# Optimization experiments

Hardware: AMD Instinct MI355X
Metric: run time of the kernel (lower is better)

Reference implementation:

```python
import jax, jax.numpy as jnp
import numpy as np


def conv1x1(x, W, b):
    # 1x1 Conv2d == per-pixel linear over channels. x: [B,C,H,W], W: [O,C], b: [O]
    return jnp.einsum('oc,bchw->bohw', W, x) + b[None, :, None, None]


def setup_inputs() -> dict:
    key = jax.random.key(0)
    ks = jax.random.split(key, 18)
    B, C, Hd, H, W = 16, 64, 64, 32, 32
    s = 0.05
    f = jax.random.normal
    return {
        'h': f(ks[0], (B, C, H, W), jnp.float32),
        'm': f(ks[1], (B, C, H, W), jnp.float32),
        'Wq': f(ks[2], (Hd, C), jnp.float32) * s,
        'bq': f(ks[3], (Hd,), jnp.float32) * s,
        'Wk': f(ks[4], (Hd, C), jnp.float32) * s,
        'bk': f(ks[5], (Hd,), jnp.float32) * s,
        'Wk2': f(ks[6], (Hd, C), jnp.float32) * s,
        'bk2': f(ks[7], (Hd,), jnp.float32) * s,
        'Wv': f(ks[8], (C, C), jnp.float32) * s,
        'bv': f(ks[9], (C,), jnp.float32) * s,
        'Wv2': f(ks[10], (C, C), jnp.float32) * s,
        'bv2': f(ks[11], (C,), jnp.float32) * s,
        'Wz': f(ks[12], (2 * C, 2 * C), jnp.float32) * s,
        'bz': f(ks[13], (2 * C,), jnp.float32) * s,
        'Wm': f(ks[14], (3 * C, 3 * C), jnp.float32) * s,
        'bm': f(ks[15], (3 * C,), jnp.float32) * s,
    }


def reference(h, m, Wq, bq, Wk, bk, Wk2, bk2, Wv, bv, Wv2, bv2, Wz, bz, Wm, bm):
    B, C, H, W = h.shape
    Hd = Wq.shape[0]
    N = H * W
    # Shared query from h
    Q_h = conv1x1(h, Wq, bq).reshape(B, Hd, N).transpose(0, 2, 1)  # [B,N,Hd]
    # Self-attention branch over h
    K_h = conv1x1(h, Wk, bk).reshape(B, Hd, N)                     # [B,Hd,N]
    A_h = jax.nn.softmax(jnp.einsum('bnd,bdm->bnm', Q_h, K_h), axis=-1)  # [B,N,N]
    V_h = conv1x1(h, Wv, bv).reshape(B, C, N)                      # [B,C,N]
    Z_h = jnp.einsum('bnm,bcm->bcn', A_h, V_h).reshape(B, C, H, W)
    # Cross-attention branch over memory m (same query Q_h)
    K_m = conv1x1(m, Wk2, bk2).reshape(B, Hd, N)
    A_m = jax.nn.softmax(jnp.einsum('bnd,bdm->bnm', Q_h, K_m), axis=-1)
    V_m = conv1x1(m, Wv2, bv2).reshape(B, C, N)
    Z_m = jnp.einsum('bnm,bcm->bcn', A_m, V_m).reshape(B, C, H, W)
    # Fuse and gated memory update
    Z = conv1x1(jnp.concatenate([Z_h, Z_m], axis=1), Wz, bz)       # [B,2C,H,W]
    combined = conv1x1(jnp.concatenate([Z, h], axis=1), Wm, bm)    # [B,3C,H,W]
    mo, mg, mi = combined[:, :C], combined[:, C:2 * C], combined[:, 2 * C:]
    mi = jax.nn.sigmoid(mi)
    new_m = (1 - mi) * m + mi * jnp.tanh(mg)
    new_h = jax.nn.sigmoid(mo) * new_m
    return (new_h, new_m)
```

## Files before the change

kernel.cpp:

```cpp
#include <hip/hip_runtime.h>

typedef unsigned short u16;
typedef unsigned int u32;
typedef __attribute__((ext_vector_type(8))) short bf16x8;
typedef __attribute__((ext_vector_type(4))) float f32x4;

#define MFMA(a, b, c) __builtin_amdgcn_mfma_f32_16x16x32_bf16((a), (b), (c), 0, 0, 0)

static __device__ __forceinline__ u16 f2bf(float x) {
  u32 u = __float_as_uint(x);
  u += 0x7FFFu + ((u >> 16) & 1u);
  return (u16)(u >> 16);
}
static __device__ __forceinline__ u32 packbf_t(float hi, float lo) {
  return __builtin_amdgcn_perm(__float_as_uint(hi), __float_as_uint(lo), 0x07060302u);
}
static __device__ __forceinline__ u32 packbf(float lo, float hi) {
  return (u32)f2bf(lo) | ((u32)f2bf(hi) << 16);
}

__global__ void prep_kernel(const float* __restrict__ Wq, const float* __restrict__ Wk,
                            const float* __restrict__ Wk2, const float* __restrict__ Wv,
                            const float* __restrict__ Wv2, const float* __restrict__ Wz,
                            const float* __restrict__ Wm, const float* __restrict__ bm,
                            u16* __restrict__ W5, u16* __restrict__ Wzb,
                            u16* __restrict__ Wmb, float* __restrict__ bmp) {
  const int id = blockIdx.x * 256 + threadIdx.x;
  if (id < 20480) {
    const int wi = id >> 12, e = id & 4095;
    const float* src = wi == 0 ? Wq : wi == 1 ? Wk : wi == 2 ? Wk2 : wi == 3 ? Wv : Wv2;
    W5[id] = f2bf(src[e]);
  } else if (id < 36864) {
    const int e = id - 20480;
    Wzb[e] = f2bf(Wz[e]);
  } else if (id < 73728) {
    const int e = id - 36864;
    const int p = e / 192, k = e % 192;
    const int hb2 = p / 96, r1 = p % 96, ctl = r1 / 48, r2 = r1 % 48;
    const int g = r2 >> 4, mm = r2 & 15;
    const int o = g * 64 + (hb2 * 2 + ctl) * 16 + mm;
    Wmb[p * 192 + k] = f2bf(Wm[o * 192 + k]);
  } else if (id < 73920) {
    const int p = id - 73728;
    const int hb2 = p / 96, r1 = p % 96, ctl = r1 / 48, r2 = r1 % 48;
    const int g = r2 >> 4, mm = r2 & 15;
    const int o = g * 64 + (hb2 * 2 + ctl) * 16 + mm;
    bmp[p] = bm[o];
  }
}

__global__ __launch_bounds__(256) void proj_kernel(
    const float* __restrict__ h, const float* __restrict__ m_,
    const float* __restrict__ bq, const float* __restrict__ bk,
    const float* __restrict__ bk2, const float* __restrict__ bv,
    const float* __restrict__ bv2, const u16* __restrict__ W5,
    u16* __restrict__ Qb, u16* __restrict__ Khb, u16* __restrict__ Kmb,
    u16* __restrict__ Vhb, u16* __restrict__ Vmb, u16* __restrict__ hbuf)
{
  const int b = blockIdx.y, n0 = blockIdx.x * 64, z = blockIdx.z;
  __shared__ __align__(16) u16 xt[64][72];
  const int tid = threadIdx.x;
  const float* __restrict__ X = z ? m_ : h;

  {
    const int px = tid & 63, c0 = (tid >> 6) * 16;
#pragma unroll
    for (int i = 0; i < 8; ++i) {
      const int c = c0 + 2 * i;
      const float f0 = X[(b * 64 + c) * 1024 + n0 + px];
      const float f1 = X[(b * 64 + c + 1) * 1024 + n0 + px];
      *(u32*)&xt[px][c] = packbf(f0, f1);
    }
  }
  __syncthreads();

  const int lane = tid & 63, w = tid >> 6;
  const int mm = lane & 15, q = lane >> 4;

  const bf16x8 xa0 = *(const bf16x8*)&xt[w * 16 + mm][q * 8];
  const bf16x8 xa1 = *(const bf16x8*)&xt[w * 16 + mm][32 + q * 8];

  auto qk_store = [&](u16* dst, const u16* Wb, const float* bias) {
#pragma unroll
    for (int ot = 0; ot < 4; ++ot) {
      const bf16x8 wb0 = *(const bf16x8*)(Wb + (ot * 16 + mm) * 64 + q * 8);
      const bf16x8 wb1 = *(const bf16x8*)(Wb + (ot * 16 + mm) * 64 + 32 + q * 8);
      const float4 b4 = *(const float4*)(bias + ot * 16 + q * 4);
      f32x4 d = {b4.x, b4.y, b4.z, b4.w};
      d = MFMA(wb0, xa0, d);
      d = MFMA(wb1, xa1, d);
      uint2 val;
      val.x = packbf(d[0], d[1]);
      val.y = packbf(d[2], d[3]);
      *(uint2*)(dst + (b * 1024 + n0 + w * 16 + mm) * 64 + ot * 16 + q * 4) = val;
    }
  };
  auto v_store = [&](u16* dst, const u16* Wb, const float* bias) {
#pragma unroll
    for (int ot = 0; ot < 4; ++ot) {
      const bf16x8 wb0 = *(const bf16x8*)(Wb + (ot * 16 + mm) * 64 + q * 8);
      const bf16x8 wb1 = *(const bf16x8*)(Wb + (ot * 16 + mm) * 64 + 32 + q * 8);
      const float bb = bias[ot * 16 + mm];
      f32x4 d = {bb, bb, bb, bb};
      d = MFMA(xa0, wb0, d);
      d = MFMA(xa1, wb1, d);
      uint2 val;
      val.x = packbf(d[0], d[1]);
      val.y = packbf(d[2], d[3]);
      *(uint2*)(dst + (b * 64 + ot * 16 + mm) * 1024 + n0 + w * 16 + q * 4) = val;
    }
  };

  if (z == 0) {
    qk_store(Qb, W5, bq);
    qk_store(Khb, W5 + 4096, bk);
    v_store(Vhb, W5 + 3 * 4096, bv);
    const int px = tid >> 2, sg = tid & 3;
    u32* dst = (u32*)(hbuf + (b * 1024 + n0 + px) * 64 + sg * 16);
    const u16* srcr = &xt[px][sg * 16];
#pragma unroll
    for (int j = 0; j < 8; ++j) dst[j] = *(const u32*)(srcr + 2 * j);
  } else {
    qk_store(Kmb, W5 + 2 * 4096, bk2);
    v_store(Vmb, W5 + 4 * 4096, bv2);
  }
}

__global__ __launch_bounds__(256, 4) void attn_kernel(
    const u16* __restrict__ Qb, const u16* __restrict__ Khb,
    const u16* __restrict__ Kmb, const u16* __restrict__ Vhb,
    const u16* __restrict__ Vmb, u16* __restrict__ Ztb)
{
  const int id = blockIdx.x;
  const int b = id & 15, rest = id >> 4;
  const int br = rest & 1, qb0 = (rest >> 1) * 32;
  const u16* __restrict__ K = br ? Kmb : Khb;
  const u16* __restrict__ V = br ? Vmb : Vhb;

  __shared__ __align__(16) u16 zcb[4][32][68];
  __shared__ float rsw[4][32];

  const int tid = threadIdx.x, w = tid >> 6, lane = tid & 63;
  const int mm = lane & 15, q = lane >> 4;

  bf16x8 qa0[2], qa1[2];
#pragma unroll
  for (int qt = 0; qt < 2; ++qt) {
    const u16* Qp = Qb + (b * 1024 + qb0 + qt * 16 + mm) * 64;
    qa0[qt] = *(const bf16x8*)(Qp + q * 8);
    qa1[qt] = *(const bf16x8*)(Qp + 32 + q * 8);
  }

  f32x4 z[2][4];
#pragma unroll
  for (int qt = 0; qt < 2; ++qt)
#pragma unroll
    for (int ct = 0; ct < 4; ++ct) z[qt][ct] = (f32x4){0.f, 0.f, 0.f, 0.f};
  float rp[2] = {0.f, 0.f};

  const int kb0 = w * 256;
  const int base = (2 * (q & 1)) * 16 + mm;
  const bool hiq = q >= 2;

  for (int ch = 0; ch < 8; ++ch) {
    const int kb = kb0 + ch * 32;
    bf16x8 kf0[2], kf1[2], vf[4];
#pragma unroll
    for (int t = 0; t < 2; ++t) {
      const u16* Kp = K + (b * 1024 + kb + t * 16 + mm) * 64;
      kf0[t] = *(const bf16x8*)(Kp + q * 8);
      kf1[t] = *(const bf16x8*)(Kp + 32 + q * 8);
    }
#pragma unroll
    for (int ct = 0; ct < 4; ++ct)
      vf[ct] = *(const bf16x8*)(V + (b * 64 + ct * 16 + mm) * 1024 + kb + q * 8);

#pragma unroll
    for (int qt = 0; qt < 2; ++qt) {
      u32 P0, P1, P2, P3;
      {
        f32x4 s = {0.f, 0.f, 0.f, 0.f};
        s = MFMA(kf0[0], qa0[qt], s);
        s = MFMA(kf1[0], qa1[qt], s);
        const float e0 = __expf(s[0]), e1 = __expf(s[1]);
        const float e2 = __expf(s[2]), e3 = __expf(s[3]);
        rp[qt] += (e0 + e1) + (e2 + e3);
        P0 = packbf_t(e1, e0);
        P1 = packbf_t(e3, e2);
      }
      {
        f32x4 s = {0.f, 0.f, 0.f, 0.f};
        s = MFMA(kf0[1], qa0[qt], s);
        s = MFMA(kf1[1], qa1[qt], s);
        const float e0 = __expf(s[0]), e1 = __expf(s[1]);
        const float e2 = __expf(s[2]), e3 = __expf(s[3]);
        rp[qt] += (e0 + e1) + (e2 + e3);
        P2 = packbf_t(e1, e0);
        P3 = packbf_t(e3, e2);
      }
      const u32 l0 = (u32)__shfl((int)P0, base),      h0 = (u32)__shfl((int)P2, base);
      const u32 l1 = (u32)__shfl((int)P1, base),      h1 = (u32)__shfl((int)P3, base);
      const u32 l2 = (u32)__shfl((int)P0, base + 16), h2 = (u32)__shfl((int)P2, base + 16);
      const u32 l3 = (u32)__shfl((int)P1, base + 16), h3 = (u32)__shfl((int)P3, base + 16);
      union { u32 u[4]; bf16x8 v; } bu;
      bu.u[0] = hiq ? h0 : l0;
      bu.u[1] = hiq ? h1 : l1;
      bu.u[2] = hiq ? h2 : l2;
      bu.u[3] = hiq ? h3 : l3;
#pragma unroll
      for (int ct = 0; ct < 4; ++ct) z[qt][ct] = MFMA(vf[ct], bu.v, z[qt][ct]);
    }
  }

#pragma unroll
  for (int qt = 0; qt < 2; ++qt) {
#pragma unroll
    for (int ct = 0; ct < 4; ++ct) {
      uint2 val;
      val.x = packbf_t(z[qt][ct][1], z[qt][ct][0]);
      val.y = packbf_t(z[qt][ct][3], z[qt][ct][2]);
      *(uint2*)&zcb[w][qt * 16 + mm][ct * 16 + q * 4] = val;
    }
    float v = rp[qt];
    v += __shfl_xor(v, 16);
    v += __shfl_xor(v, 32);
    if (q == 0) rsw[w][qt * 16 + mm] = v;
  }
  __syncthreads();

  const int c2 = tid & 31, q0 = tid >> 5;
#pragma unroll
  for (int i = 0; i < 4; ++i) {
    const int query = q0 + i * 8;
    const float rt = rsw[0][query] + rsw[1][query] + rsw[2][query] + rsw[3][query];
    const float rinv = __builtin_amdgcn_rcpf(rt);
    float vlo = 0.f, vhi = 0.f;
#pragma unroll
    for (int ww = 0; ww < 4; ++ww) {
      const u32 u = *(const u32*)&zcb[ww][query][c2 * 2];
      vlo += __uint_as_float(u << 16);
      vhi += __uint_as_float(u & 0xffff0000u);
    }
    vlo *= rinv;
    vhi *= rinv;
    *(u32*)(Ztb + (b * 1024 + qb0 + query) * 128 + br * 64 + c2 * 2) = packbf_t(vhi, vlo);
  }
}

__global__ __launch_bounds__(256) void tail_kernel(
    const u16* __restrict__ Ztb, const u16* __restrict__ hbuf,
    const float* __restrict__ m_, const u16* __restrict__ Wzb,
    const float* __restrict__ bz, const u16* __restrict__ Wmb,
    const float* __restrict__ bmp, float* __restrict__ out)
{
  const int b = blockIdx.y, n0 = blockIdx.x * 32;
  __shared__ __align__(16) u16 zp[32][136];
  const int tid = threadIdx.x, lane = tid & 63, wv = tid >> 6;
  const int mm = lane & 15, q = lane >> 4;
  const int pxt = wv & 1, oh = wv >> 1;

  {
    bf16x8 za[4];
#pragma unroll
    for (int ks = 0; ks < 4; ++ks)
      za[ks] = *(const bf16x8*)(Ztb + (b * 1024 + n0 + pxt * 16 + mm) * 128 +
                                ks * 32 + q * 8);
#pragma unroll
    for (int ot = 0; ot < 4; ++ot) {
      const int o0 = oh * 64 + ot * 16;
      const float4 b4 = *(const float4*)(bz + o0 + q * 4);
      f32x4 d = {b4.x, b4.y, b4.z, b4.w};
#pragma unroll
      for (int ks = 0; ks < 4; ++ks) {
        const bf16x8 wb = *(const bf16x8*)(Wzb + (o0 + mm) * 128 + ks * 32 + q * 8);
        d = MFMA(wb, za[ks], d);
      }
      uint2 val;
      val.x = packbf(d[0], d[1]);
      val.y = packbf(d[2], d[3]);
      *(uint2*)&zp[pxt * 16 + mm][o0 + q * 4] = val;
    }
  }
  __syncthreads();

  {
    const int hb2 = oh;
    bf16x8 fa[6];
#pragma unroll
    for (int ks = 0; ks < 4; ++ks)
      fa[ks] = *(const bf16x8*)&zp[pxt * 16 + mm][ks * 32 + q * 8];
    {
      const u16* hp = hbuf + (b * 1024 + n0 + pxt * 16 + mm) * 64;
      fa[4] = *(const bf16x8*)(hp + q * 8);
      fa[5] = *(const bf16x8*)(hp + 32 + q * 8);
    }
    f32x4 dd[6];
#pragma unroll
    for (int j = 0; j < 6; ++j) {
      const int p = hb2 * 96 + j * 16 + mm;
      const float bb = bmp[p];
      f32x4 d = {bb, bb, bb, bb};
#pragma unroll
      for (int ks = 0; ks < 6; ++ks) {
        const bf16x8 wb = *(const bf16x8*)(Wmb + p * 192 + ks * 32 + q * 8);
        d = MFMA(fa[ks], wb, d);
      }
      dd[j] = d;
    }
#pragma unroll
    for (int ctl = 0; ctl < 2; ++ctl) {
      const int c = (hb2 * 2 + ctl) * 16 + mm;
      const int px = n0 + pxt * 16 + q * 4;
      const float4 mold = *(const float4*)(m_ + (b * 64 + c) * 1024 + px);
      float4 nh, nm;
#pragma unroll
      for (int r = 0; r < 4; ++r) {
        const float xo = dd[ctl * 3 + 0][r];
        const float xg = dd[ctl * 3 + 1][r];
        const float xi = dd[ctl * 3 + 2][r];
        const float si = __builtin_amdgcn_rcpf(1.f + __expf(-xi));
        const float th = 1.f - 2.f * __builtin_amdgcn_rcpf(__expf(2.f * xg) + 1.f);
        const float so = __builtin_amdgcn_rcpf(1.f + __expf(-xo));
        const float mo = ((const float*)&mold)[r];
        const float nmv = (1.f - si) * mo + si * th;
        ((float*)&nm)[r] = nmv;
        ((float*)&nh)[r] = so * nmv;
      }
      *(float4*)(out + (b * 64 + c) * 1024 + px) = nh;
      *(float4*)(out + 1048576 + (b * 64 + c) * 1024 + px) = nm;
    }
  }
}

extern "C" void kernel_launch(void* const* d_in, const int* in_sizes, int n_in,
                              void* d_out, int out_size, void* d_ws, size_t ws_size,
                              hipStream_t stream) {
  const float* h   = (const float*)d_in[0];
  const float* m   = (const float*)d_in[1];
  const float* Wq  = (const float*)d_in[2];
  const float* bq  = (const float*)d_in[3];
  const float* Wk  = (const float*)d_in[4];
  const float* bk  = (const float*)d_in[5];
  const float* Wk2 = (const float*)d_in[6];
  const float* bk2 = (const float*)d_in[7];
  const float* Wv  = (const float*)d_in[8];
  const float* bv  = (const float*)d_in[9];
  const float* Wv2 = (const float*)d_in[10];
  const float* bv2 = (const float*)d_in[11];
  const float* Wz  = (const float*)d_in[12];
  const float* bz  = (const float*)d_in[13];
  const float* Wm  = (const float*)d_in[14];
  const float* bm  = (const float*)d_in[15];
  float* out = (float*)d_out;

  char* ws = (char*)d_ws;
  const size_t MB = 1024 * 1024;
  u16* Qb   = (u16*)(ws + 0 * MB);
  u16* Khb  = (u16*)(ws + 2 * MB);
  u16* Kmb  = (u16*)(ws + 4 * MB);
  u16* Vhb  = (u16*)(ws + 6 * MB);
  u16* Vmb  = (u16*)(ws + 8 * MB);
  u16* hbuf = (u16*)(ws + 10 * MB);
  u16* Ztb  = (u16*)(ws + 12 * MB);
  u16* W5   = (u16*)(ws + 16 * MB);
  u16* Wzb  = (u16*)(ws + 16 * MB + 40960);
  u16* Wmb  = (u16*)(ws + 16 * MB + 73728);
  float* bmp = (float*)(ws + 16 * MB + 147456);

  prep_kernel<<<289, 256, 0, stream>>>(Wq, Wk, Wk2, Wv, Wv2, Wz, Wm, bm,
                                       W5, Wzb, Wmb, bmp);
  proj_kernel<<<dim3(16, 16, 2), 256, 0, stream>>>(h, m, bq, bk, bk2, bv, bv2, W5,
                                                   Qb, Khb, Kmb, Vhb, Vmb, hbuf);
  attn_kernel<<<1024, 256, 0, stream>>>(Qb, Khb, Kmb, Vhb, Vmb, Ztb);
  tail_kernel<<<dim3(32, 16), 256, 0, stream>>>(Ztb, hbuf, m, Wzb, bz, Wmb, bmp, out);
}
```

Baseline: 157.7 us.

## Give each attention wave full key range and double-buffer K/V chunk loads

The attention kernel used to split the key range across four waves and combine partial results through shared memory with a block barrier. Now each wave owns 16 queries and walks all 1024 keys, so the LDS reduction and __syncthreads go away and the output is normalised and written straight from registers. K/V fragments are software-pipelined with two register chunks so loads overlap the MFMA and exp work. In exchange, K/V loads per query are less shared (one query tile per wave instead of two), the grid halves to 512 blocks, and the occupancy hint is dropped, which may change register allocation.

Result: slower. 178.4 us (+13.1%).

```diff
diff --git a/kernel.cpp b/kernel.cpp
--- a/kernel.cpp
+++ b/kernel.cpp
@@ -126,124 +126,102 @@
   }
 }
 
-__global__ __launch_bounds__(256, 4) void attn_kernel(
+struct Chunk { bf16x8 f[8]; };
+
+__global__ __launch_bounds__(256) void attn_kernel(
     const u16* __restrict__ Qb, const u16* __restrict__ Khb,
     const u16* __restrict__ Kmb, const u16* __restrict__ Vhb,
     const u16* __restrict__ Vmb, u16* __restrict__ Ztb)
 {
   const int id = blockIdx.x;
-  const int b = id & 15, rest = id >> 4;
-  const int br = rest & 1, qb0 = (rest >> 1) * 32;
+  const int b = id & 15;
+  const int br = (id >> 4) & 1;
+  const int qt = id >> 5;
   const u16* __restrict__ K = br ? Kmb : Khb;
   const u16* __restrict__ V = br ? Vmb : Vhb;
 
-  __shared__ __align__(16) u16 zcb[4][32][68];
-  __shared__ float rsw[4][32];
-
   const int tid = threadIdx.x, w = tid >> 6, lane = tid & 63;
   const int mm = lane & 15, q = lane >> 4;
-
-  bf16x8 qa0[2], qa1[2];
-#pragma unroll
-  for (int qt = 0; qt < 2; ++qt) {
-    const u16* Qp = Qb + (b * 1024 + qb0 + qt * 16 + mm) * 64;
-    qa0[qt] = *(const bf16x8*)(Qp + q * 8);
-    qa1[qt] = *(const bf16x8*)(Qp + 32 + q * 8);
-  }
-
-  f32x4 z[2][4];
-#pragma unroll
-  for (int qt = 0; qt < 2; ++qt)
-#pragma unroll
-    for (int ct = 0; ct < 4; ++ct) z[qt][ct] = (f32x4){0.f, 0.f, 0.f, 0.f};
-  float rp[2] = {0.f, 0.f};
-
-  const int kb0 = w * 256;
+  const int q0 = qt * 64 + w * 16;
+
+  const u16* Qp = Qb + (b * 1024 + q0 + mm) * 64;
+  const bf16x8 qa0 = *(const bf16x8*)(Qp + q * 8);
+  const bf16x8 qa1 = *(const bf16x8*)(Qp + 32 + q * 8);
+
+  f32x4 z[4];
+#pragma unroll
+  for (int ct = 0; ct < 4; ++ct) z[ct] = (f32x4){0.f, 0.f, 0.f, 0.f};
+  float rp = 0.f;
+
   const int base = (2 * (q & 1)) * 16 + mm;
   const bool hiq = q >= 2;
 
-  for (int ch = 0; ch < 8; ++ch) {
-    const int kb = kb0 + ch * 32;
-    bf16x8 kf0[2], kf1[2], vf[4];
-#pragma unroll
-    for (int t = 0; t < 2; ++t) {
-      const u16* Kp = K + (b * 1024 + kb + t * 16 + mm) * 64;
-      kf0[t] = *(const bf16x8*)(Kp + q * 8);
-      kf1[t] = *(const bf16x8*)(Kp + 32 + q * 8);
-    }
+  auto loadch = [&](int kb, Chunk& c) {
+    const u16* Kp0 = K + (b * 1024 + kb + mm) * 64;
+    c.f[0] = *(const bf16x8*)(Kp0 + q * 8);
+    c.f[1] = *(const bf16x8*)(Kp0 + 32 + q * 8);
+    c.f[2] = *(const bf16x8*)(Kp0 + 1024 + q * 8);
+    c.f[3] = *(const bf16x8*)(Kp0 + 1024 + 32 + q * 8);
 #pragma unroll
     for (int ct = 0; ct < 4; ++ct)
-      vf[ct] = *(const bf16x8*)(V + (b * 64 + ct * 16 + mm) * 1024 + kb + q * 8);
-
-#pragma unroll
-    for (int qt = 0; qt < 2; ++qt) {
-      u32 P0, P1, P2, P3;
-      {
-        f32x4 s = {0.f, 0.f, 0.f, 0.f};
-        s = MFMA(kf0[0], qa0[qt], s);
-        s = MFMA(kf1[0], qa1[qt], s);
-        const float e0 = __expf(s[0]), e1 = __expf(s[1]);
-        const float e2 = __expf(s[2]), e3 = __expf(s[3]);
-        rp[qt] += (e0 + e1) + (e2 + e3);
-        P0 = packbf_t(e1, e0);
-        P1 = packbf_t(e3, e2);
-      }
-      {
-        f32x4 s = {0.f, 0.f, 0.f, 0.f};
-        s = MFMA(kf0[1], qa0[qt], s);
-        s = MFMA(kf1[1], qa1[qt], s);
-        const float e0 = __expf(s[0]), e1 = __expf(s[1]);
-        const float e2 = __expf(s[2]), e3 = __expf(s[3]);
-        rp[qt] += (e0 + e1) + (e2 + e3);
-        P2 = packbf_t(e1, e0);
-        P3 = packbf_t(e3, e2);
-      }
-      const u32 l0 = (u32)__shfl((int)P0, base),      h0 = (u32)__shfl((int)P2, base);
-      const u32 l1 = (u32)__shfl((int)P1, base),      h1 = (u32)__shfl((int)P3, base);
-      const u32 l2 = (u32)__shfl((int)P0, base + 16), h2 = (u32)__shfl((int)P2, base + 16);
-      const u32 l3 = (u32)__shfl((int)P1, base + 16), h3 = (u32)__shfl((int)P3, base + 16);
-      union { u32 u[4]; bf16x8 v; } bu;
-      bu.u[0] = hiq ? h0 : l0;
-      bu.u[1] = hiq ? h1 : l1;
-      bu.u[2] = hiq ? h2 : l2;
-      bu.u[3] = hiq ? h3 : l3;
-#pragma unroll
-      for (int ct = 0; ct < 4; ++ct) z[qt][ct] = MFMA(vf[ct], bu.v, z[qt][ct]);
-    }
-  }
-
-#pragma unroll
-  for (int qt = 0; qt < 2; ++qt) {
-#pragma unroll
-    for (int ct = 0; ct < 4; ++ct) {
-      uint2 val;
-      val.x = packbf_t(z[qt][ct][1], z[qt][ct][0]);
-      val.y = packbf_t(z[qt][ct][3], z[qt][ct][2]);
-      *(uint2*)&zcb[w][qt * 16 + mm][ct * 16 + q * 4] = val;
-    }
-    float v = rp[qt];
-    v += __shfl_xor(v, 16);
-    v += __shfl_xor(v, 32);
-    if (q == 0) rsw[w][qt * 16 + mm] = v;
-  }
-  __syncthreads();
-
-  const int c2 = tid & 31, q0 = tid >> 5;
-#pragma unroll
-  for (int i = 0; i < 4; ++i) {
-    const int query = q0 + i * 8;
-    const float rt = rsw[0][query] + rsw[1][query] + rsw[2][query] + rsw[3][query];
-    const float rinv = __builtin_amdgcn_rcpf(rt);
-    float vlo = 0.f, vhi = 0.f;
-#pragma unroll
-    for (int ww = 0; ww < 4; ++ww) {
-      const u32 u = *(const u32*)&zcb[ww][query][c2 * 2];
-      vlo += __uint_as_float(u << 16);
-      vhi += __uint_as_float(u & 0xffff0000u);
-    }
-    vlo *= rinv;
-    vhi *= rinv;
-    *(u32*)(Ztb + (b * 1024 + qb0 + query) * 128 + br * 64 + c2 * 2) = packbf_t(vhi, vlo);
+      c.f[4 + ct] = *(const bf16x8*)(V + (b * 64 + ct * 16 + mm) * 1024 + kb + q * 8);
+  };
+
+  auto compute = [&](const Chunk& c) {
+    u32 P0, P1, P2, P3;
+    {
+      f32x4 s = {0.f, 0.f, 0.f, 0.f};
+      s = MFMA(c.f[0], qa0, s);
+      s = MFMA(c.f[1], qa1, s);
+      const float e0 = __expf(s[0]), e1 = __expf(s[1]);
+      const float e2 = __expf(s[2]), e3 = __expf(s[3]);
+      rp += (e0 + e1) + (e2 + e3);
+      P0 = packbf_t(e1, e0);
+      P1 = packbf_t(e3, e2);
+    }
+    {
+      f32x4 s = {0.f, 0.f, 0.f, 0.f};
+      s = MFMA(c.f[2], qa0, s);
+      s = MFMA(c.f[3], qa1, s);
+      const float e0 = __expf(s[0]), e1 = __expf(s[1]);
+      const float e2 = __expf(s[2]), e3 = __expf(s[3]);
+      rp += (e0 + e1) + (e2 + e3);
+      P2 = packbf_t(e1, e0);
+      P3 = packbf_t(e3, e2);
+    }
+    const u32 l0 = (u32)__shfl((int)P0, base),      h0 = (u32)__shfl((int)P2, base);
+    const u32 l1 = (u32)__shfl((int)P1, base),      h1 = (u32)__shfl((int)P3, base);
+    const u32 l2 = (u32)__shfl((int)P0, base + 16), h2 = (u32)__shfl((int)P2, base + 16);
+    const u32 l3 = (u32)__shfl((int)P1, base + 16), h3 = (u32)__shfl((int)P3, base + 16);
+    union { u32 u[4]; bf16x8 v; } bu;
+    bu.u[0] = hiq ? h0 : l0;
+    bu.u[1] = hiq ? h1 : l1;
+    bu.u[2] = hiq ? h2 : l2;
+    bu.u[3] = hiq ? h3 : l3;
+#pragma unroll
+    for (int ct = 0; ct < 4; ++ct) z[ct] = MFMA(c.f[4 + ct], bu.v, z[ct]);
+  };
+
+  Chunk fA, fB;
+  loadch(0, fA);
+#pragma unroll 1
+  for (int cc = 0; cc < 16; ++cc) {
+    loadch(cc * 64 + 32, fB);
+    compute(fA);
+    if (cc < 15) loadch(cc * 64 + 64, fA);
+    compute(fB);
+  }
+
+  rp += __shfl_xor(rp, 16);
+  rp += __shfl_xor(rp, 32);
+  const float rinv = __builtin_amdgcn_rcpf(rp);
+  u16* Zr = Ztb + (b * 1024 + q0 + mm) * 128 + br * 64 + q * 4;
+#pragma unroll
+  for (int ct = 0; ct < 4; ++ct) {
+    uint2 val;
+    val.x = packbf(z[ct][0] * rinv, z[ct][1] * rinv);
+    val.y = packbf(z[ct][2] * rinv, z[ct][3] * rinv);
+    *(uint2*)(Zr + ct * 16) = val;
   }
 }
 
@@ -371,6 +349,6 @@
                                        W5, Wzb, Wmb, bmp);
   proj_kernel<<<dim3(16, 16, 2), 256, 0, stream>>>(h, m, bq, bk, bk2, bv, bv2, W5,
                                                    Qb, Khb, Kmb, Vhb, Vmb, hbuf);
-  attn_kernel<<<1024, 256, 0, stream>>>(Qb, Khb, Kmb, Vhb, Vmb, Ztb);
+  attn_kernel<<<512, 256, 0, stream>>>(Qb, Khb, Kmb, Vhb, Vmb, Ztb);
   tail_kernel<<<dim3(32, 16), 256, 0, stream>>>(Ztb, hbuf, m, Wzb, bz, Wmb, bmp, out);
 }
```

## Restructure attention to share K/V tiles via double-buffered LDS across query waves

Applied to the files above, without the earlier changes.

Attention blocks now give each wave its own 32 queries over the full key range, instead of splitting keys across waves and reducing partial sums through LDS at the end. K and V chunks of 64 keys are staged cooperatively into swizzled, double-buffered shared memory with register prefetch, so four waves reuse each loaded tile. The V projection layout is changed to key-chunk-major tiles to match, and P is transposed through a small LDS scratch instead of cross-lane shuffles. The grid drops from 1024 to 256 blocks, which lowers parallelism on the device and adds a barrier per chunk.

After: 141.7 us. 10.2% less time.

```diff
diff --git a/kernel.cpp b/kernel.cpp
--- a/kernel.cpp
+++ b/kernel.cpp
@@ -107,7 +107,8 @@
       uint2 val;
       val.x = packbf(d[0], d[1]);
       val.y = packbf(d[2], d[3]);
-      *(uint2*)(dst + (b * 64 + ot * 16 + mm) * 1024 + n0 + w * 16 + q * 4) = val;
+      *(uint2*)(dst + b * 65536 + blockIdx.x * 4096 + (ot * 16 + mm) * 64 +
+                w * 16 + q * 4) = val;
     }
   };
 
@@ -126,27 +127,30 @@
   }
 }
 
-__global__ __launch_bounds__(256, 4) void attn_kernel(
+__global__ __launch_bounds__(256) void attn_kernel(
     const u16* __restrict__ Qb, const u16* __restrict__ Khb,
     const u16* __restrict__ Kmb, const u16* __restrict__ Vhb,
     const u16* __restrict__ Vmb, u16* __restrict__ Ztb)
 {
   const int id = blockIdx.x;
-  const int b = id & 15, rest = id >> 4;
-  const int br = rest & 1, qb0 = (rest >> 1) * 32;
-  const u16* __restrict__ K = br ? Kmb : Khb;
-  const u16* __restrict__ V = br ? Vmb : Vhb;
-
-  __shared__ __align__(16) u16 zcb[4][32][68];
-  __shared__ float rsw[4][32];
+  const int b = id & 15;
+  const int br = (id >> 4) & 1;
+  const int qh = id >> 5;
+  const u16* __restrict__ K = (br ? Kmb : Khb) + b * 65536;
+  const u16* __restrict__ V = (br ? Vmb : Vhb) + b * 65536;
+
+  __shared__ __align__(16) u16 Kl[2][4096];
+  __shared__ __align__(16) u16 Vl[2][4096];
+  __shared__ __align__(16) u16 ps[4][16][40];
 
   const int tid = threadIdx.x, w = tid >> 6, lane = tid & 63;
-  const int mm = lane & 15, q = lane >> 4;
+  const int mm = lane & 15, q = lane >> 4, m7 = mm & 7;
+  const int q0 = qh * 128 + w * 32;
 
   bf16x8 qa0[2], qa1[2];
 #pragma unroll
   for (int qt = 0; qt < 2; ++qt) {
-    const u16* Qp = Qb + (b * 1024 + qb0 + qt * 16 + mm) * 64;
+    const u16* Qp = Qb + (b * 1024 + q0 + qt * 16 + mm) * 64;
     qa0[qt] = *(const bf16x8*)(Qp + q * 8);
     qa1[qt] = *(const bf16x8*)(Qp + 32 + q * 8);
   }
@@ -158,92 +162,93 @@
     for (int ct = 0; ct < 4; ++ct) z[qt][ct] = (f32x4){0.f, 0.f, 0.f, 0.f};
   float rp[2] = {0.f, 0.f};
 
-  const int kb0 = w * 256;
-  const int base = (2 * (q & 1)) * 16 + mm;
-  const bool hiq = q >= 2;
-
-  for (int ch = 0; ch < 8; ++ch) {
-    const int kb = kb0 + ch * 32;
-    bf16x8 kf0[2], kf1[2], vf[4];
-#pragma unroll
-    for (int t = 0; t < 2; ++t) {
-      const u16* Kp = K + (b * 1024 + kb + t * 16 + mm) * 64;
-      kf0[t] = *(const bf16x8*)(Kp + q * 8);
-      kf1[t] = *(const bf16x8*)(Kp + 32 + q * 8);
-    }
-#pragma unroll
-    for (int ct = 0; ct < 4; ++ct)
-      vf[ct] = *(const bf16x8*)(V + (b * 64 + ct * 16 + mm) * 1024 + kb + q * 8);
-
-#pragma unroll
-    for (int qt = 0; qt < 2; ++qt) {
-      u32 P0, P1, P2, P3;
-      {
-        f32x4 s = {0.f, 0.f, 0.f, 0.f};
-        s = MFMA(kf0[0], qa0[qt], s);
-        s = MFMA(kf1[0], qa1[qt], s);
-        const float e0 = __expf(s[0]), e1 = __expf(s[1]);
-        const float e2 = __expf(s[2]), e3 = __expf(s[3]);
-        rp[qt] += (e0 + e1) + (e2 + e3);
-        P0 = packbf_t(e1, e0);
-        P1 = packbf_t(e3, e2);
-      }
-      {
-        f32x4 s = {0.f, 0.f, 0.f, 0.f};
-        s = MFMA(kf0[1], qa0[qt], s);
-        s = MFMA(kf1[1], qa1[qt], s);
-        const float e0 = __expf(s[0]), e1 = __expf(s[1]);
-        const float e2 = __expf(s[2]), e3 = __expf(s[3]);
-        rp[qt] += (e0 + e1) + (e2 + e3);
-        P2 = packbf_t(e1, e0);
-        P3 = packbf_t(e3, e2);
-      }
-      const u32 l0 = (u32)__shfl((int)P0, base),      h0 = (u32)__shfl((int)P2, base);
-      const u32 l1 = (u32)__shfl((int)P1, base),      h1 = (u32)__shfl((int)P3, base);
-      const u32 l2 = (u32)__shfl((int)P0, base + 16), h2 = (u32)__shfl((int)P2, base + 16);
-      const u32 l3 = (u32)__shfl((int)P1, base + 16), h3 = (u32)__shfl((int)P3, base + 16);
-      union { u32 u[4]; bf16x8 v; } bu;
-      bu.u[0] = hiq ? h0 : l0;
-      bu.u[1] = hiq ? h1 : l1;
-      bu.u[2] = hiq ? h2 : l2;
-      bu.u[3] = hiq ? h3 : l3;
-#pragma unroll
-      for (int ct = 0; ct < 4; ++ct) z[qt][ct] = MFMA(vf[ct], bu.v, z[qt][ct]);
-    }
+  const int u0 = tid, u1 = 256 + tid;
+  const int l0 = (((u0 & ~7) | ((u0 ^ (u0 >> 3)) & 7))) * 8;
+  const int l1 = (((u1 & ~7) | ((u1 ^ (u1 >> 3)) & 7))) * 8;
+  uint4 sk0, sk1, sv0, sv1;
+
+  auto stage_load = [&](int kc) {
+    const u16* Ks = K + kc * 4096;
+    const u16* Vs = V + kc * 4096;
+    sk0 = *(const uint4*)(Ks + u0 * 8);
+    sk1 = *(const uint4*)(Ks + u1 * 8);
+    sv0 = *(const uint4*)(Vs + u0 * 8);
+    sv1 = *(const uint4*)(Vs + u1 * 8);
+  };
+  auto stage_store = [&](u16* Kd, u16* Vd) {
+    *(uint4*)(Kd + l0) = sk0;
+    *(uint4*)(Kd + l1) = sk1;
+    *(uint4*)(Vd + l0) = sv0;
+    *(uint4*)(Vd + l1) = sv1;
+  };
+
+  stage_load(0);
+  stage_store(Kl[0], Vl[0]);
+  __syncthreads();
+
+  const u16* Kcur = Kl[0];
+  const u16* Vcur = Vl[0];
+  u16* Knxt = Kl[1];
+  u16* Vnxt = Vl[1];
+
+#pragma unroll 1
+  for (int kc = 0; kc < 16; ++kc) {
+    if (kc < 15) stage_load(kc + 1);
+
+#pragma unroll
+    for (int t2 = 0; t2 < 2; ++t2) {
+      bf16x8 kf0[2], kf1[2], vf[4];
+#pragma unroll
+      for (int tt = 0; tt < 2; ++tt) {
+        const u16* Kb = Kcur + (t2 * 32 + tt * 16 + mm) * 64;
+        kf0[tt] = *(const bf16x8*)(Kb + ((q ^ m7) * 8));
+        kf1[tt] = *(const bf16x8*)(Kb + (((q + 4) ^ m7) * 8));
+      }
+#pragma unroll
+      for (int ct = 0; ct < 4; ++ct) {
+        const u16* Vb = Vcur + (ct * 16 + mm) * 64;
+        vf[ct] = *(const bf16x8*)(Vb + (((t2 * 4 + q) ^ m7) * 8));
+      }
+
+#pragma unroll
+      for (int qt = 0; qt < 2; ++qt) {
+#pragma unroll
+        for (int tt = 0; tt < 2; ++tt) {
+          f32x4 s = {0.f, 0.f, 0.f, 0.f};
+          s = MFMA(kf0[tt], qa0[qt], s);
+          s = MFMA(kf1[tt], qa1[qt], s);
+          const float e0 = __expf(s[0]), e1 = __expf(s[1]);
+          const float e2 = __expf(s[2]), e3 = __expf(s[3]);
+          rp[qt] += (e0 + e1) + (e2 + e3);
+          *(u32*)&ps[w][mm][tt * 16 + q * 4] = packbf_t(e1, e0);
+          *(u32*)&ps[w][mm][tt * 16 + q * 4 + 2] = packbf_t(e3, e2);
+        }
+        const bf16x8 pb = *(const bf16x8*)&ps[w][mm][q * 8];
+#pragma unroll
+        for (int ct = 0; ct < 4; ++ct) z[qt][ct] = MFMA(vf[ct], pb, z[qt][ct]);
+      }
+    }
+
+    if (kc < 15) stage_store(Knxt, Vnxt);
+    __syncthreads();
+    const u16* tk = Kcur; Kcur = Knxt; Knxt = (u16*)tk;
+    const u16* tv = Vcur; Vcur = Vnxt; Vnxt = (u16*)tv;
   }
 
 #pragma unroll
   for (int qt = 0; qt < 2; ++qt) {
-#pragma unroll
-    for (int ct = 0; ct < 4; ++ct) {
-      uint2 val;
-      val.x = packbf_t(z[qt][ct][1], z[qt][ct][0]);
-      val.y = packbf_t(z[qt][ct][3], z[qt][ct][2]);
-      *(uint2*)&zcb[w][qt * 16 + mm][ct * 16 + q * 4] = val;
-    }
     float v = rp[qt];
     v += __shfl_xor(v, 16);
     v += __shfl_xor(v, 32);
-    if (q == 0) rsw[w][qt * 16 + mm] = v;
-  }
-  __syncthreads();
-
-  const int c2 = tid & 31, q0 = tid >> 5;
-#pragma unroll
-  for (int i = 0; i < 4; ++i) {
-    const int query = q0 + i * 8;
-    const float rt = rsw[0][query] + rsw[1][query] + rsw[2][query] + rsw[3][query];
-    const float rinv = __builtin_amdgcn_rcpf(rt);
-    float vlo = 0.f, vhi = 0.f;
-#pragma unroll
-    for (int ww = 0; ww < 4; ++ww) {
-      const u32 u = *(const u32*)&zcb[ww][query][c2 * 2];
-      vlo += __uint_as_float(u << 16);
-      vhi += __uint_as_float(u & 0xffff0000u);
-    }
-    vlo *= rinv;
-    vhi *= rinv;
-    *(u32*)(Ztb + (b * 1024 + qb0 + query) * 128 + br * 64 + c2 * 2) = packbf_t(vhi, vlo);
+    const float rinv = __builtin_amdgcn_rcpf(v);
+    u16* Zr = Ztb + (b * 1024 + q0 + qt * 16 + mm) * 128 + br * 64;
+#pragma unroll
+    for (int ct = 0; ct < 4; ++ct) {
+      uint2 val;
+      val.x = packbf(z[qt][ct][0] * rinv, z[qt][ct][1] * rinv);
+      val.y = packbf(z[qt][ct][2] * rinv, z[qt][ct][3] * rinv);
+      *(uint2*)(Zr + ct * 16 + q * 4) = val;
+    }
   }
 }
 
@@ -371,6 +376,6 @@
                                        W5, Wzb, Wmb, bmp);
   proj_kernel<<<dim3(16, 16, 2), 256, 0, stream>>>(h, m, bq, bk, bk2, bv, bv2, W5,
                                                    Qb, Khb, Kmb, Vhb, Vmb, hbuf);
-  attn_kernel<<<1024, 256, 0, stream>>>(Qb, Khb, Kmb, Vhb, Vmb, Ztb);
+  attn_kernel<<<256, 256, 0, stream>>>(Qb, Khb, Kmb, Vhb, Vmb, Ztb);
   tail_kernel<<<dim3(32, 16), 256, 0, stream>>>(Ztb, hbuf, m, Wzb, bz, Wmb, bmp, out);
 }
```
